# Performance work log

Hardware: AMD Instinct MI355X
Metric: run time of the kernel (lower is better)

Reference implementation:

```python
import jax, jax.numpy as jnp
import numpy as np

N_NODES = 10000
N_EDGES = 320000
IN_DIM = 256
OUT_DIM = 256
LN_EPS = 1e-5


def setup_inputs() -> dict:
    key = jax.random.key(0)
    ks = jax.random.split(key, 4)
    x = jax.random.normal(ks[0], (N_NODES, IN_DIM), dtype=jnp.float32)
    edge_index = jax.random.randint(ks[1], (2, N_EDGES), 0, N_NODES, dtype=jnp.int64)
    # Linear weights stored input-major so y = x @ W + b
    W_msg = jax.random.normal(ks[2], (2 * IN_DIM, OUT_DIM), dtype=jnp.float32) / np.sqrt(2 * IN_DIM)
    b_msg = jnp.zeros((OUT_DIM,), dtype=jnp.float32)
    W_upd = jax.random.normal(ks[3], (IN_DIM + OUT_DIM, OUT_DIM), dtype=jnp.float32) / np.sqrt(IN_DIM + OUT_DIM)
    b_upd = jnp.zeros((OUT_DIM,), dtype=jnp.float32)
    gamma = jnp.ones((OUT_DIM,), dtype=jnp.float32)
    beta = jnp.zeros((OUT_DIM,), dtype=jnp.float32)
    return {"x": x, "edge_index": edge_index, "W_msg": W_msg, "b_msg": b_msg,
            "W_upd": W_upd, "b_upd": b_upd, "gamma": gamma, "beta": beta}


def reference(x, edge_index, W_msg, b_msg, W_upd, b_upd, gamma, beta):
    row, col = edge_index[0], edge_index[1]
    # gather -> concat -> linear -> relu   [E, out_dim]
    msg_in = jnp.concatenate([x[row], x[col]], axis=-1)
    messages = jax.nn.relu(msg_in @ W_msg + b_msg)
    # scatter-add aggregate over destination nodes  [N, out_dim]
    aggregated = jax.ops.segment_sum(messages, col, num_segments=x.shape[0])
    # update: concat -> linear -> relu -> layernorm
    h = jax.nn.relu(jnp.concatenate([x, aggregated], axis=-1) @ W_upd + b_upd)
    mu = jnp.mean(h, axis=-1, keepdims=True)
    var = jnp.mean(jnp.square(h - mu), axis=-1, keepdims=True)
    return (h - mu) * jax.lax.rsqrt(var + LN_EPS) * gamma + beta
```

## Files before the change

kernel.cpp:

```cpp
#include <hip/hip_runtime.h>
#include <hip/hip_bf16.h>
#include <stdint.h>

#define NNODES 10000
#define NEDGES 320000
#define DIM    256
#define KTOT   512
#define LN_EPS 1e-5f
#define BCAP   96

typedef __attribute__((ext_vector_type(4))) float f32x4;
typedef __attribute__((ext_vector_type(8))) short bf16x8;

__device__ __forceinline__ ushort f2bf(float f) {
    union { float f; uint32_t u; } v; v.f = f;
    uint32_t r = v.u + 0x7fffu + ((v.u >> 16) & 1u);
    return (ushort)(r >> 16);
}
__device__ __forceinline__ float bf2f(ushort u) {
    union { float f; uint32_t u; } v; v.u = ((uint32_t)u) << 16;
    return v.f;
}

__global__ __launch_bounds__(256)
void prep_all(const float* __restrict__ x, const float* __restrict__ Wm,
              const float* __restrict__ Wu, ushort* __restrict__ xb,
              ushort* __restrict__ Wcat, ushort* __restrict__ Wua,
              int4* __restrict__ cntz) {
    int tid = blockIdx.x * 256 + threadIdx.x;
    if (tid < 2560) cntz[tid] = (int4){0, 0, 0, 0};
    if (tid < 640000) {
        float4 v = reinterpret_cast<const float4*>(x)[tid];
        ushort4 o;
        o.x = f2bf(v.x); o.y = f2bf(v.y); o.z = f2bf(v.z); o.w = f2bf(v.w);
        reinterpret_cast<ushort4*>(xb)[tid] = o;
    } else {
        int t = tid - 640000;
        if (t < 131072) {
            int kk  = t >> 14;
            int rem = t & 16383;
            int g   = rem >> 9;
            int kg  = (rem >> 7) & 3;
            int ml  = (rem >> 3) & 15;
            int j   = rem & 7;
            int k = kk * 32 + kg * 8 + j;
            int n = g * 16 + ml;
            float v = (n < 256) ? Wm[k * DIM + n] : Wm[(k + 256) * DIM + (n - 256)];
            Wcat[t] = f2bf(v);
        } else {
            int rem = t - 131072;
            int kk  = rem >> 13;
            int nt  = (rem >> 9) & 15;
            int kg  = (rem >> 7) & 3;
            int ml  = (rem >> 3) & 15;
            int j   = rem & 7;
            int k = kk * 32 + kg * 8 + j;
            int n = nt * 16 + ml;
            Wua[rem] = f2bf(Wu[k * DIM + n]);
        }
    }
}

__global__ __launch_bounds__(256)
void scatter_uv(const int* __restrict__ eidx, int* __restrict__ cnt,
                int* __restrict__ srow, const ushort* __restrict__ xb,
                const ushort* __restrict__ Wcat, const float* __restrict__ bmsg,
                ushort* __restrict__ Ub, float* __restrict__ Vf) {
    if (blockIdx.x < 1250) {
        int e = blockIdx.x * 256 + threadIdx.x;
        int d = eidx[NEDGES + e];
        int p = atomicAdd(&cnt[d], 1);
        if (p < BCAP) srow[d * BCAP + p] = eidx[e];
        return;
    }
    const int wq   = threadIdx.x >> 6;
    const int lane = threadIdx.x & 63;
    const int ml = lane & 15, kg = lane >> 4;
    const int nb = (blockIdx.x - 1250) * 16;
    const uint arow = (uint)(nb + ml) * DIM;

    f32x4 acc[8];
#pragma unroll
    for (int nt = 0; nt < 8; ++nt) acc[nt] = (f32x4){0.f, 0.f, 0.f, 0.f};

#pragma unroll
    for (int kk = 0; kk < 8; ++kk) {
        bf16x8 a = *reinterpret_cast<const bf16x8*>(xb + arow + kk * 32 + kg * 8);
#pragma unroll
        for (int nt = 0; nt < 8; ++nt) {
            bf16x8 b = *reinterpret_cast<const bf16x8*>(Wcat + kk * 16384 + (wq * 8 + nt) * 512 + lane * 8);
            acc[nt] = __builtin_amdgcn_mfma_f32_16x16x32_bf16(a, b, acc[nt], 0, 0, 0);
        }
    }

    if (wq < 2) {
#pragma unroll
        for (int nt = 0; nt < 8; ++nt) {
            const int col = wq * 128 + nt * 16 + ml;
#pragma unroll
            for (int i = 0; i < 4; ++i)
                Ub[(size_t)(nb + kg * 4 + i) * 256 + col] = f2bf(acc[nt][i]);
        }
    } else {
#pragma unroll
        for (int nt = 0; nt < 8; ++nt) {
            const int col = (wq - 2) * 128 + nt * 16 + ml;
            const float bb = bmsg[col];
#pragma unroll
            for (int i = 0; i < 4; ++i)
                Vf[(size_t)(nb + kg * 4 + i) * 256 + col] = acc[nt][i] + bb;
        }
    }
}

__global__ __launch_bounds__(512)
void edge_node(const ushort* __restrict__ Ub, const float* __restrict__ Vf,
               const int* __restrict__ srow, const int* __restrict__ cnt,
               const ushort* __restrict__ xb, const ushort* __restrict__ Wua,
               const float* __restrict__ bupd, const float* __restrict__ gamma,
               const float* __restrict__ beta, float* __restrict__ out) {
    __shared__ float aggS[16][260];
    __shared__ float pS[16][8][2];

    const int tid  = threadIdx.x;
    const int wave = tid >> 6, lane = tid & 63;
    const int nb = blockIdx.x * 16;
    const int el = lane >> 5;
    const int cl = lane & 31;
    const int c0 = cl * 8;

#pragma unroll
    for (int nn = 0; nn < 2; ++nn) {
        const int d = nb + wave * 2 + nn;
        int deg = cnt[d]; deg = deg < BCAP ? deg : BCAP;
        const int beg = d * BCAP;
        const float4 va = *reinterpret_cast<const float4*>(&Vf[(size_t)d * 256 + c0]);
        const float4 vb = *reinterpret_cast<const float4*>(&Vf[(size_t)d * 256 + c0 + 4]);
        float s[8];
#pragma unroll
        for (int j = 0; j < 8; ++j) s[j] = 0.f;

#define ACC8(U) do { \
        s[0] += fmaxf(bf2f((ushort)(U)[0]) + va.x, 0.f); \
        s[1] += fmaxf(bf2f((ushort)(U)[1]) + va.y, 0.f); \
        s[2] += fmaxf(bf2f((ushort)(U)[2]) + va.z, 0.f); \
        s[3] += fmaxf(bf2f((ushort)(U)[3]) + va.w, 0.f); \
        s[4] += fmaxf(bf2f((ushort)(U)[4]) + vb.x, 0.f); \
        s[5] += fmaxf(bf2f((ushort)(U)[5]) + vb.y, 0.f); \
        s[6] += fmaxf(bf2f((ushort)(U)[6]) + vb.z, 0.f); \
        s[7] += fmaxf(bf2f((ushort)(U)[7]) + vb.w, 0.f); } while (0)

        int i = el;
        for (; i + 6 < deg; i += 8) {
            int r0 = srow[beg + i],     r1 = srow[beg + i + 2];
            int r2 = srow[beg + i + 4], r3 = srow[beg + i + 6];
            bf16x8 u0 = *reinterpret_cast<const bf16x8*>(&Ub[(size_t)r0 * 256 + c0]);
            bf16x8 u1 = *reinterpret_cast<const bf16x8*>(&Ub[(size_t)r1 * 256 + c0]);
            bf16x8 u2 = *reinterpret_cast<const bf16x8*>(&Ub[(size_t)r2 * 256 + c0]);
            bf16x8 u3 = *reinterpret_cast<const bf16x8*>(&Ub[(size_t)r3 * 256 + c0]);
            ACC8(u0); ACC8(u1); ACC8(u2); ACC8(u3);
        }
        for (; i < deg; i += 2) {
            int r = srow[beg + i];
            bf16x8 u = *reinterpret_cast<const bf16x8*>(&Ub[(size_t)r * 256 + c0]);
            ACC8(u);
        }
#undef ACC8
#pragma unroll
        for (int j = 0; j < 8; ++j) s[j] += __shfl_xor(s[j], 32);
        if (el == 0) {
            *reinterpret_cast<float4*>(&aggS[wave * 2 + nn][c0])     = (float4){s[0], s[1], s[2], s[3]};
            *reinterpret_cast<float4*>(&aggS[wave * 2 + nn][c0 + 4]) = (float4){s[4], s[5], s[6], s[7]};
        }
    }
    __syncthreads();

    const int ml = lane & 15, kg = lane >> 4, wq = wave;
    const uint arow = (uint)(nb + ml) * DIM;

    f32x4 acc[2];
    acc[0] = (f32x4){0.f, 0.f, 0.f, 0.f};
    acc[1] = (f32x4){0.f, 0.f, 0.f, 0.f};

#pragma unroll
    for (int kk = 0; kk < 8; ++kk) {
        bf16x8 a = *reinterpret_cast<const bf16x8*>(xb + arow + kk * 32 + kg * 8);
#pragma unroll
        for (int nt = 0; nt < 2; ++nt) {
            bf16x8 b = *reinterpret_cast<const bf16x8*>(Wua + kk * 8192 + (wq * 2 + nt) * 512 + lane * 8);
            acc[nt] = __builtin_amdgcn_mfma_f32_16x16x32_bf16(a, b, acc[nt], 0, 0, 0);
        }
    }
#pragma unroll
    for (int kk = 0; kk < 8; ++kk) {
        float4 f0 = *reinterpret_cast<const float4*>(&aggS[ml][kk * 32 + kg * 8]);
        float4 f1 = *reinterpret_cast<const float4*>(&aggS[ml][kk * 32 + kg * 8 + 4]);
        union { bf16x8 v; __hip_bfloat162 h2[4]; } u;
        u.h2[0] = __float22bfloat162_rn(make_float2(f0.x, f0.y));
        u.h2[1] = __float22bfloat162_rn(make_float2(f0.z, f0.w));
        u.h2[2] = __float22bfloat162_rn(make_float2(f1.x, f1.y));
        u.h2[3] = __float22bfloat162_rn(make_float2(f1.z, f1.w));
#pragma unroll
        for (int nt = 0; nt < 2; ++nt) {
            bf16x8 b = *reinterpret_cast<const bf16x8*>(Wua + 65536 + kk * 8192 + (wq * 2 + nt) * 512 + lane * 8);
            acc[nt] = __builtin_amdgcn_mfma_f32_16x16x32_bf16(u.v, b, acc[nt], 0, 0, 0);
        }
    }

    float sum[4] = {0.f, 0.f, 0.f, 0.f}, ssq[4] = {0.f, 0.f, 0.f, 0.f};
#pragma unroll
    for (int nt = 0; nt < 2; ++nt) {
        const float bb = bupd[(wq * 2 + nt) * 16 + ml];
#pragma unroll
        for (int i = 0; i < 4; ++i) {
            float v = acc[nt][i] + bb;
            v = v > 0.f ? v : 0.f;
            acc[nt][i] = v;
            sum[i] += v;
            ssq[i] += v * v;
        }
    }
#pragma unroll
    for (int m = 1; m < 16; m <<= 1) {
#pragma unroll
        for (int i = 0; i < 4; ++i) {
            sum[i] += __shfl_xor(sum[i], m);
            ssq[i] += __shfl_xor(ssq[i], m);
        }
    }
    if (ml == 0) {
#pragma unroll
        for (int i = 0; i < 4; ++i) {
            pS[kg * 4 + i][wq][0] = sum[i];
            pS[kg * 4 + i][wq][1] = ssq[i];
        }
    }
    __syncthreads();

    float mu[4], rs[4];
#pragma unroll
    for (int i = 0; i < 4; ++i) {
        int r = kg * 4 + i;
        float S = 0.f, Q = 0.f;
#pragma unroll
        for (int w = 0; w < 8; ++w) { S += pS[r][w][0]; Q += pS[r][w][1]; }
        float m = S * (1.f / 256.f);
        float var = Q * (1.f / 256.f) - m * m;
        mu[i] = m;
        rs[i] = rsqrtf(var + LN_EPS);
    }
#pragma unroll
    for (int nt = 0; nt < 2; ++nt) {
        const int cc = (wq * 2 + nt) * 16 + ml;
        const float g = gamma[cc], be = beta[cc];
#pragma unroll
        for (int i = 0; i < 4; ++i) {
            const int node = nb + kg * 4 + i;
            out[(size_t)node * DIM + cc] = (acc[nt][i] - mu[i]) * rs[i] * g + be;
        }
    }
}

extern "C" void kernel_launch(void* const* d_in, const int* in_sizes, int n_in,
                              void* d_out, int out_size, void* d_ws, size_t ws_size,
                              hipStream_t stream) {
    const float* x    = (const float*)d_in[0];
    const int*   eidx = (const int*)  d_in[1];
    const float* Wm   = (const float*)d_in[2];
    const float* bm   = (const float*)d_in[3];
    const float* Wu   = (const float*)d_in[4];
    const float* bu   = (const float*)d_in[5];
    const float* gam  = (const float*)d_in[6];
    const float* bet  = (const float*)d_in[7];
    float* out = (float*)d_out;

    char* ws = (char*)d_ws;
    ushort* xb     = (ushort*)(ws);
    ushort* Ub     = (ushort*)(ws +  5120000);
    float*  Vf     = (float*) (ws + 10240000);
    ushort* Wcat   = (ushort*)(ws + 20480000);
    ushort* Wua    = (ushort*)(ws + 20742144);
    int*    cnt    = (int*)   (ws + 21004288);
    int*    srow   = (int*)   (ws + 21045248);

    prep_all<<<3524, 256, 0, stream>>>(x, Wm, Wu, xb, Wcat, Wua, (int4*)cnt);
    scatter_uv<<<1875, 256, 0, stream>>>(eidx, cnt, srow, xb, Wcat, bm, Ub, Vf);
    edge_node<<<625, 512, 0, stream>>>(Ub, Vf, srow, cnt, xb, Wua, bu, gam, bet, out);
}
```

Before: 83.66 us.

## Spread each node's edge aggregation across all waves by column slice

```diff
diff --git a/kernel.cpp b/kernel.cpp
--- a/kernel.cpp
+++ b/kernel.cpp
@@ -119,58 +119,46 @@
                const ushort* __restrict__ xb, const ushort* __restrict__ Wua,
                const float* __restrict__ bupd, const float* __restrict__ gamma,
                const float* __restrict__ beta, float* __restrict__ out) {
-    __shared__ float aggS[16][260];
+    __shared__ float aggB[4096];
     __shared__ float pS[16][8][2];
 
     const int tid  = threadIdx.x;
     const int wave = tid >> 6, lane = tid & 63;
     const int nb = blockIdx.x * 16;
-    const int el = lane >> 5;
-    const int cl = lane & 31;
-    const int c0 = cl * 8;
-
-#pragma unroll
-    for (int nn = 0; nn < 2; ++nn) {
-        const int d = nb + wave * 2 + nn;
+    const int slot = lane >> 3;
+    const int cg   = lane & 7;
+    const int c0   = wave * 32 + cg * 4;
+
+    for (int nn = 0; nn < 16; ++nn) {
+        const int d = nb + nn;
         int deg = cnt[d]; deg = deg < BCAP ? deg : BCAP;
         const int beg = d * BCAP;
-        const float4 va = *reinterpret_cast<const float4*>(&Vf[(size_t)d * 256 + c0]);
-        const float4 vb = *reinterpret_cast<const float4*>(&Vf[(size_t)d * 256 + c0 + 4]);
-        float s[8];
-#pragma unroll
-        for (int j = 0; j < 8; ++j) s[j] = 0.f;
-
-#define ACC8(U) do { \
-        s[0] += fmaxf(bf2f((ushort)(U)[0]) + va.x, 0.f); \
-        s[1] += fmaxf(bf2f((ushort)(U)[1]) + va.y, 0.f); \
-        s[2] += fmaxf(bf2f((ushort)(U)[2]) + va.z, 0.f); \
-        s[3] += fmaxf(bf2f((ushort)(U)[3]) + va.w, 0.f); \
-        s[4] += fmaxf(bf2f((ushort)(U)[4]) + vb.x, 0.f); \
-        s[5] += fmaxf(bf2f((ushort)(U)[5]) + vb.y, 0.f); \
-        s[6] += fmaxf(bf2f((ushort)(U)[6]) + vb.z, 0.f); \
-        s[7] += fmaxf(bf2f((ushort)(U)[7]) + vb.w, 0.f); } while (0)
-
-        int i = el;
-        for (; i + 6 < deg; i += 8) {
-            int r0 = srow[beg + i],     r1 = srow[beg + i + 2];
-            int r2 = srow[beg + i + 4], r3 = srow[beg + i + 6];
-            bf16x8 u0 = *reinterpret_cast<const bf16x8*>(&Ub[(size_t)r0 * 256 + c0]);
-            bf16x8 u1 = *reinterpret_cast<const bf16x8*>(&Ub[(size_t)r1 * 256 + c0]);
-            bf16x8 u2 = *reinterpret_cast<const bf16x8*>(&Ub[(size_t)r2 * 256 + c0]);
-            bf16x8 u3 = *reinterpret_cast<const bf16x8*>(&Ub[(size_t)r3 * 256 + c0]);
-            ACC8(u0); ACC8(u1); ACC8(u2); ACC8(u3);
-        }
-        for (; i < deg; i += 2) {
-            int r = srow[beg + i];
-            bf16x8 u = *reinterpret_cast<const bf16x8*>(&Ub[(size_t)r * 256 + c0]);
-            ACC8(u);
-        }
-#undef ACC8
-#pragma unroll
-        for (int j = 0; j < 8; ++j) s[j] += __shfl_xor(s[j], 32);
-        if (el == 0) {
-            *reinterpret_cast<float4*>(&aggS[wave * 2 + nn][c0])     = (float4){s[0], s[1], s[2], s[3]};
-            *reinterpret_cast<float4*>(&aggS[wave * 2 + nn][c0 + 4]) = (float4){s[4], s[5], s[6], s[7]};
+        const float4 vc = *reinterpret_cast<const float4*>(&Vf[(size_t)d * 256 + c0]);
+        float s0 = 0.f, s1 = 0.f, s2 = 0.f, s3 = 0.f;
+
+        const int iters = (deg + 7) >> 3;
+        for (int it = 0; it < iters; ++it) {
+            const int ei = it * 8 + slot;
+            const bool ok = ei < deg;
+            const int r = ok ? srow[beg + ei] : 0;
+            ushort4 u = *reinterpret_cast<const ushort4*>(&Ub[(size_t)r * 256 + c0]);
+            if (ok) {
+                s0 += fmaxf(bf2f(u.x) + vc.x, 0.f);
+                s1 += fmaxf(bf2f(u.y) + vc.y, 0.f);
+                s2 += fmaxf(bf2f(u.z) + vc.z, 0.f);
+                s3 += fmaxf(bf2f(u.w) + vc.w, 0.f);
+            }
+        }
+#pragma unroll
+        for (int m = 8; m < 64; m <<= 1) {
+            s0 += __shfl_xor(s0, m);
+            s1 += __shfl_xor(s1, m);
+            s2 += __shfl_xor(s2, m);
+            s3 += __shfl_xor(s3, m);
+        }
+        if (slot == 0) {
+            const int idx = wave * 512 + (cg >> 1) * 128 + nn * 8 + (cg & 1) * 4;
+            *reinterpret_cast<float4*>(&aggB[idx]) = (float4){s0, s1, s2, s3};
         }
     }
     __syncthreads();
@@ -193,8 +181,9 @@
     }
 #pragma unroll
     for (int kk = 0; kk < 8; ++kk) {
-        float4 f0 = *reinterpret_cast<const float4*>(&aggS[ml][kk * 32 + kg * 8]);
-        float4 f1 = *reinterpret_cast<const float4*>(&aggS[ml][kk * 32 + kg * 8 + 4]);
+        const int idx = kk * 512 + kg * 128 + ml * 8;
+        float4 f0 = *reinterpret_cast<const float4*>(&aggB[idx]);
+        float4 f1 = *reinterpret_cast<const float4*>(&aggB[idx + 4]);
         union { bf16x8 v; __hip_bfloat162 h2[4]; } u;
         u.h2[0] = __float22bfloat162_rn(make_float2(f0.x, f0.y));
         u.h2[1] = __float22bfloat162_rn(make_float2(f0.z, f0.w));
```

Measured after the change: 116.4 us. 1.39x slower.

## Halve nodes per block in edge_node and deepen gather unroll

Applied to the files above, without the earlier changes.

```diff
diff --git a/kernel.cpp b/kernel.cpp
--- a/kernel.cpp
+++ b/kernel.cpp
@@ -119,19 +119,18 @@
                const ushort* __restrict__ xb, const ushort* __restrict__ Wua,
                const float* __restrict__ bupd, const float* __restrict__ gamma,
                const float* __restrict__ beta, float* __restrict__ out) {
-    __shared__ float aggS[16][260];
+    __shared__ float aggS[8][260];
     __shared__ float pS[16][8][2];
 
     const int tid  = threadIdx.x;
     const int wave = tid >> 6, lane = tid & 63;
-    const int nb = blockIdx.x * 16;
+    const int nb = blockIdx.x * 8;
     const int el = lane >> 5;
     const int cl = lane & 31;
     const int c0 = cl * 8;
 
-#pragma unroll
-    for (int nn = 0; nn < 2; ++nn) {
-        const int d = nb + wave * 2 + nn;
+    {
+        const int d = nb + wave;
         int deg = cnt[d]; deg = deg < BCAP ? deg : BCAP;
         const int beg = d * BCAP;
         const float4 va = *reinterpret_cast<const float4*>(&Vf[(size_t)d * 256 + c0]);
@@ -151,14 +150,16 @@
         s[7] += fmaxf(bf2f((ushort)(U)[7]) + vb.w, 0.f); } while (0)
 
         int i = el;
-        for (; i + 6 < deg; i += 8) {
-            int r0 = srow[beg + i],     r1 = srow[beg + i + 2];
-            int r2 = srow[beg + i + 4], r3 = srow[beg + i + 6];
-            bf16x8 u0 = *reinterpret_cast<const bf16x8*>(&Ub[(size_t)r0 * 256 + c0]);
-            bf16x8 u1 = *reinterpret_cast<const bf16x8*>(&Ub[(size_t)r1 * 256 + c0]);
-            bf16x8 u2 = *reinterpret_cast<const bf16x8*>(&Ub[(size_t)r2 * 256 + c0]);
-            bf16x8 u3 = *reinterpret_cast<const bf16x8*>(&Ub[(size_t)r3 * 256 + c0]);
-            ACC8(u0); ACC8(u1); ACC8(u2); ACC8(u3);
+        for (; i + 14 < deg; i += 16) {
+            int r[8];
+#pragma unroll
+            for (int j = 0; j < 8; ++j) r[j] = srow[beg + i + 2 * j];
+            bf16x8 u[8];
+#pragma unroll
+            for (int j = 0; j < 8; ++j)
+                u[j] = *reinterpret_cast<const bf16x8*>(&Ub[(size_t)r[j] * 256 + c0]);
+#pragma unroll
+            for (int j = 0; j < 8; ++j) ACC8(u[j]);
         }
         for (; i < deg; i += 2) {
             int r = srow[beg + i];
@@ -169,14 +170,13 @@
 #pragma unroll
         for (int j = 0; j < 8; ++j) s[j] += __shfl_xor(s[j], 32);
         if (el == 0) {
-            *reinterpret_cast<float4*>(&aggS[wave * 2 + nn][c0])     = (float4){s[0], s[1], s[2], s[3]};
-            *reinterpret_cast<float4*>(&aggS[wave * 2 + nn][c0 + 4]) = (float4){s[4], s[5], s[6], s[7]};
-        }
-    }
-    __syncthreads();
+            *reinterpret_cast<float4*>(&aggS[wave][c0])     = (float4){s[0], s[1], s[2], s[3]};
+            *reinterpret_cast<float4*>(&aggS[wave][c0 + 4]) = (float4){s[4], s[5], s[6], s[7]};
+        }
+    }
 
     const int ml = lane & 15, kg = lane >> 4, wq = wave;
-    const uint arow = (uint)(nb + ml) * DIM;
+    const uint arow = (uint)(nb + (ml & 7)) * DIM;
 
     f32x4 acc[2];
     acc[0] = (f32x4){0.f, 0.f, 0.f, 0.f};
@@ -191,10 +191,12 @@
             acc[nt] = __builtin_amdgcn_mfma_f32_16x16x32_bf16(a, b, acc[nt], 0, 0, 0);
         }
     }
+    __syncthreads();
+
 #pragma unroll
     for (int kk = 0; kk < 8; ++kk) {
-        float4 f0 = *reinterpret_cast<const float4*>(&aggS[ml][kk * 32 + kg * 8]);
-        float4 f1 = *reinterpret_cast<const float4*>(&aggS[ml][kk * 32 + kg * 8 + 4]);
+        float4 f0 = *reinterpret_cast<const float4*>(&aggS[ml & 7][kk * 32 + kg * 8]);
+        float4 f1 = *reinterpret_cast<const float4*>(&aggS[ml & 7][kk * 32 + kg * 8 + 4]);
         union { bf16x8 v; __hip_bfloat162 h2[4]; } u;
         u.h2[0] = __float22bfloat162_rn(make_float2(f0.x, f0.y));
         u.h2[1] = __float22bfloat162_rn(make_float2(f0.z, f0.w));
@@ -249,14 +251,16 @@
         mu[i] = m;
         rs[i] = rsqrtf(var + LN_EPS);
     }
-#pragma unroll
-    for (int nt = 0; nt < 2; ++nt) {
-        const int cc = (wq * 2 + nt) * 16 + ml;
-        const float g = gamma[cc], be = beta[cc];
-#pragma unroll
-        for (int i = 0; i < 4; ++i) {
-            const int node = nb + kg * 4 + i;
-            out[(size_t)node * DIM + cc] = (acc[nt][i] - mu[i]) * rs[i] * g + be;
+    if (kg < 2) {
+#pragma unroll
+        for (int nt = 0; nt < 2; ++nt) {
+            const int cc = (wq * 2 + nt) * 16 + ml;
+            const float g = gamma[cc], be = beta[cc];
+#pragma unroll
+            for (int i = 0; i < 4; ++i) {
+                const int node = nb + kg * 4 + i;
+                out[(size_t)node * DIM + cc] = (acc[nt][i] - mu[i]) * rs[i] * g + be;
+            }
         }
     }
 }
@@ -285,5 +289,5 @@
 
     prep_all<<<3524, 256, 0, stream>>>(x, Wm, Wu, xb, Wcat, Wua, (int4*)cnt);
     scatter_uv<<<1875, 256, 0, stream>>>(eidx, cnt, srow, xb, Wcat, bm, Ub, Vf);
-    edge_node<<<625, 512, 0, stream>>>(Ub, Vf, srow, cnt, xb, Wua, bu, gam, bet, out);
-}
+    edge_node<<<NNODES / 8, 512, 0, stream>>>(Ub, Vf, srow, cnt, xb, Wua, bu, gam, bet, out);
+}
```

After: 88.22 us. 1.05x slower.
